# Kernel tuning notes

Hardware: AMD Instinct MI355X
Metric: run time of the kernel (lower is better)

Reference implementation:

```python
import jax, jax.numpy as jnp
import numpy as np


def setup_inputs() -> dict:
    key = jax.random.key(0)
    ks = jax.random.split(key, 6)
    m, d, n, p = 4096, 1024, 16, 1024  # tokens, input_dim, num_experts, output_dim (=slots)
    h = (d + p) * 2 // 3  # 1365, hidden_dim per original module
    s = 0.02
    return {
        "x": jax.random.normal(ks[0], (m, d), jnp.float32),
        "phi": jax.random.normal(ks[1], (d, n, p), jnp.float32) * s,
        "W1": jax.random.normal(ks[2], (n, d, h), jnp.float32) * s,
        "b1": jax.random.normal(ks[3], (n, h), jnp.float32) * s,
        "W2": jax.random.normal(ks[4], (n, h, p), jnp.float32) * s,
        "b2": jax.random.normal(ks[5], (n, p), jnp.float32) * s,
    }


def reference(x, phi, W1, b1, W2, b2):
    # logits: [m, n, p] = tokens x experts x slots
    logits = jnp.einsum('md,dnp->mnp', x, phi)
    # Dispatch weights: softmax over tokens' expert axis (dim=1 in torch == experts n)
    D = jax.nn.softmax(logits, axis=1)
    # Combine weights: softmax over all (expert, slot) pairs per token
    m = logits.shape[0]
    C = jax.nn.softmax(logits.reshape(m, -1), axis=-1).reshape(logits.shape)
    # Slot inputs: [n, p, d]
    Xs = jnp.einsum('md,mnp->npd', x, D)
    # Batched per-expert MLP (replaces the Python loop over experts)
    H = jax.nn.relu(jnp.einsum('npd,ndh->nph', Xs, W1) + b1[:, None, :])
    Ys = jnp.einsum('nph,nho->npo', H, W2) + b2[:, None, :]  # [n, p, out]
    # Combine: [m, out]; flatten(start_dim=1) on a 2D tensor is a no-op
    Y = jnp.einsum('npo,mnp->mo', Ys, C)
    return Y
```

## Files before the change

kernel.cpp:

```cpp
#include <hip/hip_runtime.h>
#include <math.h>

#define MTOK 4096
#define DDIM 1024
#define NEXP 16
#define PSLOT 1024
#define NPDIM 16384
#define HDIM 1365
#define HPAD 1376
#define KSPL 4

typedef unsigned short u16;
typedef __attribute__((ext_vector_type(8))) short short8;
typedef __attribute__((ext_vector_type(8))) unsigned short ushort8;
typedef __attribute__((ext_vector_type(2))) unsigned int uint32x2;
typedef __attribute__((ext_vector_type(4))) unsigned int uint32x4;
typedef __attribute__((ext_vector_type(4))) float f32x4;

template<bool Bc, typename T, typename F> struct cond_t { using type = T; };
template<typename T, typename F> struct cond_t<false, T, F> { using type = F; };

__device__ __forceinline__ float b2f(u16 v) {
    union { unsigned int u; float f; } x;
    x.u = ((unsigned int)v) << 16;
    return x.f;
}
__device__ __forceinline__ u16 f2b(float f) {
    union { float f; unsigned int u; } x;
    x.f = f;
    unsigned int r = x.u + 0x7FFFu + ((x.u >> 16) & 1u);
    return (u16)(r >> 16);
}
__device__ __forceinline__ unsigned int cvtpk(float lo, float hi) {
    unsigned int r;
    asm("v_cvt_pk_bf16_f32 %0, %1, %2" : "=v"(r) : "v"(lo), "v"(hi));
    return r;
}
__device__ __forceinline__ void stv(float* p, long long i, float v) { p[i] = v; }
__device__ __forceinline__ void stv(u16*  p, long long i, float v) { p[i] = f2b(v); }

template<int AMODE, int BMODE, typename TA, typename TB, typename TC,
         bool BIASF, bool RELUF, bool ROWSC, bool BCHK>
__global__ __launch_bounds__(512) void mgemm(
    const TA* __restrict__ A, long long sA, int lda,
    const TB* __restrict__ B, long long sB, int ldb,
    TC* __restrict__ C, long long sC, int ldc,
    const float* __restrict__ S,
    const float* __restrict__ bias, long long sBias,
    const float* __restrict__ rowsc,
    int M, int N, int NZ, int K, int Kb, int Nb)
{
    constexpr int AS = (AMODE == 0) ? 32 : 40;
    constexpr int BS = (BMODE == 0) ? 32 : 40;
    __shared__ u16 As[2][256 * AS];
    __shared__ u16 Bs[2][128 * BS];

    const int bz = blockIdx.z;
    A += (long long)bz * sA;
    B += (long long)bz * sB;
    C += (long long)bz * sC;
    const float* biasp = BIASF ? (bias + (long long)bz * sBias) : nullptr;

    const int gx = gridDim.x;
    const int nwg = gx * gridDim.y;
    int wg = blockIdx.x + gx * blockIdx.y;
    {
        const int q = nwg >> 3, r = nwg & 7, xc = wg & 7, ix = wg >> 3;
        wg = (xc < r ? xc * (q + 1) : r + xc * q) + ix;
    }
    const int m0 = (wg / gx) * 256;
    const int n0 = (wg % gx) * 128;

    const int tid  = threadIdx.x;
    const int lane = tid & 63;
    const int wv   = tid >> 6;
    const int wm   = wv & 3;
    const int wn   = wv >> 2;
    const int quad = lane >> 4;
    const int l16  = lane & 15;

    const int cla  = 2 * (tid & 127);
    const int k8a  = tid >> 7;
    const int clb  = 2 * (tid & 63);
    const int kqb  = tid >> 6;
    const int ngb  = n0 + clb;

    auto aoff = [&](int row, int k8) {
        int o = row * AS + k8 * 8;
        if constexpr (AMODE != 0) o ^= ((row >> 3) & 3) << 3;
        return o;
    };
    auto boff = [&](int row, int kel) {
        int o = row * BS + kel;
        if constexpr (BMODE != 0) o ^= ((row >> 3) & 3) << 3;
        return o;
    };

    f32x4 acc[4][4];
#pragma unroll
    for (int i = 0; i < 4; ++i)
#pragma unroll
        for (int j = 0; j < 4; ++j) acc[i][j] = (f32x4){0.f, 0.f, 0.f, 0.f};

    using BRAW = typename cond_t<sizeof(TB) == 2, unsigned int[4], float[8]>::type;

    auto LOADA0 = [&](int k0, int buf) {
#pragma unroll
        for (int q = 0; q < 2; ++q) {
            const u16* gp = A + (long long)(m0 + wv * 32 + q * 16 + (lane >> 2)) * lda
                              + k0 + (lane & 3) * 8;
            u16* lp = &As[buf][(wv * 32 + q * 16) * 32];
            __builtin_amdgcn_global_load_lds(
                (const __attribute__((address_space(1))) unsigned int*)gp,
                (__attribute__((address_space(3))) unsigned int*)lp, 16, 0, 0);
        }
    };
    auto LOADA2 = [&](int k0, unsigned int (&araw)[8], float2 (&sr)[8]) {
#pragma unroll
        for (int i = 0; i < 8; ++i) {
            const long long kg = k0 + k8a * 8 + i;
            araw[i] = *(const unsigned int*)((const u16*)A + kg * lda + (m0 + cla));
            sr[i]   = *(const float2*)&S[kg * 1024 + ((m0 + cla) & 1023)];
        }
    };
    auto WRITEA = [&](int buf, unsigned int (&araw)[8], float2 (&sr)[8]) {
        uint32x4 wa, wb;
#pragma unroll
        for (int j = 0; j < 4; ++j) {
            const unsigned int r0 = araw[2 * j], r1 = araw[2 * j + 1];
            wa[j] = cvtpk(b2f((u16)(r0 & 0xFFFFu)) * sr[2 * j].x,
                          b2f((u16)(r1 & 0xFFFFu)) * sr[2 * j + 1].x);
            wb[j] = cvtpk(b2f((u16)(r0 >> 16)) * sr[2 * j].y,
                          b2f((u16)(r1 >> 16)) * sr[2 * j + 1].y);
        }
        *(uint32x4*)&As[buf][aoff(cla, k8a)]     = wa;
        *(uint32x4*)&As[buf][aoff(cla + 1, k8a)] = wb;
    };
    auto LOADB0 = [&](int k0, int buf) {
        const u16* gp = (const u16*)B + (long long)(n0 + wv * 16 + (lane >> 2)) * ldb
                          + k0 + (lane & 3) * 8;
        u16* lp = &Bs[buf][(wv * 16) * 32];
        __builtin_amdgcn_global_load_lds(
            (const __attribute__((address_space(1))) unsigned int*)gp,
            (__attribute__((address_space(3))) unsigned int*)lp, 16, 0, 0);
    };
    auto LOADB = [&](int k0, BRAW& braw) {
        if constexpr (sizeof(TB) == 2) {
#pragma unroll
            for (int i = 0; i < 4; ++i) {
                const int kg = k0 + kqb * 4 + i;
                braw[i] = *(const unsigned int*)((const u16*)B + (long long)kg * ldb + ngb);
            }
        } else {
            bool full = true;
            if constexpr (BCHK) full = (k0 + 32 <= Kb) && (n0 + 128 <= Nb);
            if (full) {
#pragma unroll
                for (int i = 0; i < 4; ++i) {
                    const int kg = k0 + kqb * 4 + i;
                    const float* bp = (const float*)B + (long long)kg * ldb + ngb;
                    braw[2 * i]     = bp[0];
                    braw[2 * i + 1] = bp[1];
                }
            } else {
#pragma unroll
                for (int i = 0; i < 4; ++i) {
                    const int kg = k0 + kqb * 4 + i;
                    float v0 = 0.f, v1 = 0.f;
                    if (kg < Kb) {
                        if (ngb < Nb)     v0 = ((const float*)B)[(long long)kg * ldb + ngb];
                        if (ngb + 1 < Nb) v1 = ((const float*)B)[(long long)kg * ldb + ngb + 1];
                    }
                    braw[2 * i]     = v0;
                    braw[2 * i + 1] = v1;
                }
            }
        }
    };
    auto WRITEB = [&](int buf, BRAW& braw) {
        uint32x2 wa, wb;
        if constexpr (sizeof(TB) == 2) {
            wa[0] = (braw[0] & 0xFFFFu) | (braw[1] << 16);
            wa[1] = (braw[2] & 0xFFFFu) | (braw[3] << 16);
            wb[0] = (braw[0] >> 16) | (braw[1] & 0xFFFF0000u);
            wb[1] = (braw[2] >> 16) | (braw[3] & 0xFFFF0000u);
        } else {
            wa[0] = cvtpk(braw[0], braw[2]);
            wa[1] = cvtpk(braw[4], braw[6]);
            wb[0] = cvtpk(braw[1], braw[3]);
            wb[1] = cvtpk(braw[5], braw[7]);
        }
        *(uint32x2*)&Bs[buf][boff(clb, kqb * 4)]     = wa;
        *(uint32x2*)&Bs[buf][boff(clb + 1, kqb * 4)] = wb;
    };
    auto MM = [&](int buf) {
        short8 bfr[4];
#pragma unroll
        for (int ni = 0; ni < 4; ++ni)
            bfr[ni] = *(const short8*)&Bs[buf][boff(wn * 64 + ni * 16 + l16, quad * 8)];
#pragma unroll
        for (int mi = 0; mi < 4; ++mi) {
            short8 a = *(const short8*)&As[buf][aoff(wm * 64 + mi * 16 + l16, quad)];
#pragma unroll
            for (int ni = 0; ni < 4; ++ni)
                acc[mi][ni] = __builtin_amdgcn_mfma_f32_16x16x32_bf16(a, bfr[ni], acc[mi][ni], 0, 0, 0);
        }
    };

    const int nt = K >> 5;
    unsigned int a0[8];
    float2 sr[8];
    BRAW braw;
    {
        if constexpr (AMODE == 0) LOADA0(0, 0);
        else                      LOADA2(0, a0, sr);
        if constexpr (BMODE == 0) LOADB0(0, 0);
        else                      LOADB(0, braw);
        if constexpr (AMODE != 0) WRITEA(0, a0, sr);
        if constexpr (BMODE != 0) WRITEB(0, braw);
        __syncthreads();
    }
    for (int t = 0; t < nt; ++t) {
        const int cur = t & 1, nxt = cur ^ 1;
        const bool pf = (t + 1 < nt);
        if (pf) {
            if constexpr (AMODE == 0) LOADA0((t + 1) * 32, nxt);
            else                      LOADA2((t + 1) * 32, a0, sr);
            if constexpr (BMODE == 0) LOADB0((t + 1) * 32, nxt);
            else                      LOADB((t + 1) * 32, braw);
        }
        MM(cur);
        if (pf) {
            if constexpr (AMODE != 0) WRITEA(nxt, a0, sr);
            if constexpr (BMODE != 0) WRITEB(nxt, braw);
        }
        __syncthreads();
    }

#pragma unroll
    for (int mi = 0; mi < 4; ++mi) {
#pragma unroll
        for (int r = 0; r < 4; ++r) {
            const int rg = m0 + wm * 64 + mi * 16 + quad * 4 + r;
            if (rg >= M) continue;
            const float rs = ROWSC ? rowsc[rg] : 1.f;
#pragma unroll
            for (int ni = 0; ni < 4; ++ni) {
                const int cg = n0 + wn * 64 + ni * 16 + l16;
                if (cg < N) {
                    float v = acc[mi][ni][r];
                    if (BIASF) v += biasp[cg];
                    if (RELUF) v = fmaxf(v, 0.f);
                    if (ROWSC) v *= rs;
                    stv(C, (long long)rg * ldc + cg, v);
                } else if (cg < NZ) {
                    stv(C, (long long)rg * ldc + cg, 0.f);
                }
            }
        }
    }
}

__global__ __launch_bounds__(256) void cvt_k(
    const float* __restrict__ src, u16* __restrict__ dst, long long n)
{
    const long long i = ((long long)blockIdx.x * 256 + threadIdx.x) * 8;
    if (i >= n) return;
    const float4 a = *(const float4*)&src[i];
    const float4 b = *(const float4*)&src[i + 4];
    uint32x4 v;
    v[0] = cvtpk(a.x, a.y);
    v[1] = cvtpk(a.z, a.w);
    v[2] = cvtpk(b.x, b.y);
    v[3] = cvtpk(b.z, b.w);
    *(uint32x4*)&dst[i] = v;
}

__global__ __launch_bounds__(256) void tcvt_k(
    const float* __restrict__ src, u16* __restrict__ dst, int R, int C)
{
    __shared__ float t[32][33];
    const int c0 = blockIdx.x * 32, r0 = blockIdx.y * 32;
    const int tr = threadIdx.x >> 3;
    const int tc = (threadIdx.x & 7) * 4;
    const float4 v = *(const float4*)&src[(long long)(r0 + tr) * C + c0 + tc];
    t[tr][tc]     = v.x;
    t[tr][tc + 1] = v.y;
    t[tr][tc + 2] = v.z;
    t[tr][tc + 3] = v.w;
    __syncthreads();
    uint32x2 o;
    o[0] = cvtpk(t[tc][tr],     t[tc + 1][tr]);
    o[1] = cvtpk(t[tc + 2][tr], t[tc + 3][tr]);
    *(uint32x2*)&dst[(long long)(c0 + tr) * R + r0 + tc] = o;
}

__global__ __launch_bounds__(256) void softmax_k(
    u16* __restrict__ L, float* __restrict__ rsd, float* __restrict__ rsc)
{
    const int m = blockIdx.x;
    u16* row = L + (long long)m * NPDIM;
    const int tid = threadIdx.x;
    __shared__ float red[256];

    float mx = -1e30f;
    for (int i = tid * 8; i < NPDIM; i += 2048) {
        const ushort8 v = *(const ushort8*)&row[i];
#pragma unroll
        for (int j = 0; j < 8; ++j) mx = fmaxf(mx, b2f(v[j]));
    }
    red[tid] = mx;
    __syncthreads();
    for (int s = 128; s > 0; s >>= 1) {
        if (tid < s) red[tid] = fmaxf(red[tid], red[tid + s]);
        __syncthreads();
    }
    const float mxAll = red[0];
    __syncthreads();

    float sum = 0.f;
    for (int i = tid * 8; i < NPDIM; i += 2048) {
        const ushort8 v = *(const ushort8*)&row[i];
        ushort8 e;
#pragma unroll
        for (int j = 0; j < 8; ++j) {
            const float ef = __expf(b2f(v[j]) - mxAll);
            const u16 eb = f2b(ef);
            e[j] = eb;
            sum += b2f(eb);
        }
        *(ushort8*)&row[i] = e;
    }
    red[tid] = sum;
    __syncthreads();
    for (int s = 128; s > 0; s >>= 1) {
        if (tid < s) red[tid] += red[tid + s];
        __syncthreads();
    }
    if (tid == 0) rsc[m] = 1.f / red[0];
    __syncthreads();

    {
        const int p0 = tid * 4;
        float s0 = 0.f, s1 = 0.f, s2 = 0.f, s3 = 0.f;
#pragma unroll
        for (int n = 0; n < NEXP; ++n) {
            const ushort4 v = *(const ushort4*)&row[n * PSLOT + p0];
            s0 += b2f(v.x); s1 += b2f(v.y); s2 += b2f(v.z); s3 += b2f(v.w);
        }
        const float4 r = {1.f / s0, 1.f / s1, 1.f / s2, 1.f / s3};
        *(float4*)&rsd[(long long)m * PSLOT + p0] = r;
    }
}

__global__ __launch_bounds__(256) void reduce_k(
    const float* __restrict__ Yp, float* __restrict__ Y)
{
    const long long S = (long long)MTOK * PSLOT;
    const long long i = ((long long)blockIdx.x * 256 + threadIdx.x) * 4;
    f32x4 r = *(const f32x4*)&Yp[i];
#pragma unroll
    for (int z = 1; z < KSPL; ++z) r += *(const f32x4*)&Yp[(long long)z * S + i];
    *(f32x4*)&Y[i] = r;
}

extern "C" void kernel_launch(void* const* d_in, const int* in_sizes, int n_in,
                              void* d_out, int out_size, void* d_ws, size_t ws_size,
                              hipStream_t stream)
{
    const float* x   = (const float*)d_in[0];
    const float* phi = (const float*)d_in[1];
    const float* W1  = (const float*)d_in[2];
    const float* b1  = (const float*)d_in[3];
    const float* W2  = (const float*)d_in[4];
    const float* b2  = (const float*)d_in[5];
    float* Y = (float*)d_out;

    char* w = (char*)d_ws;
    u16*   L     = (u16*)w;   w += (size_t)MTOK * NPDIM * 2;
    u16*   Ys    = (u16*)w;   w += (size_t)NEXP * PSLOT * PSLOT * 2;
    float* rsc   = (float*)w; w += (size_t)MTOK * 4;
    float* Yp    = (float*)w;
    float* rsd   = (float*)w; w += (size_t)MTOK * PSLOT * 4;
    u16*   Xs    = (u16*)w;   w += (size_t)NEXP * PSLOT * DDIM * 2;
    u16*   Hb    = (u16*)w;   w += (size_t)NEXP * PSLOT * HPAD * 2;
    u16*   phibT = Ys;
    u16*   xb    = Hb;
    u16*   xbT   = Hb + (size_t)MTOK * DDIM;

    cvt_k<<<dim3((MTOK * DDIM) / (8 * 256)), 256, 0, stream>>>(x, xb, (long long)MTOK * DDIM);
    tcvt_k<<<dim3(DDIM / 32, MTOK / 32), 256, 0, stream>>>(x, xbT, MTOK, DDIM);
    tcvt_k<<<dim3(NPDIM / 32, DDIM / 32), 256, 0, stream>>>(phi, phibT, DDIM, NPDIM);

    mgemm<0, 0, u16, u16, u16, false, false, false, false>
        <<<dim3(NPDIM / 128, MTOK / 256, 1), 512, 0, stream>>>(
        xb, 0, DDIM,  phibT, 0, DDIM,  L, 0, NPDIM,
        nullptr, nullptr, 0, nullptr,
        MTOK, NPDIM, NPDIM, DDIM, DDIM, NPDIM);

    softmax_k<<<dim3(MTOK), 256, 0, stream>>>(L, rsd, rsc);

    mgemm<2, 0, u16, u16, u16, false, false, false, false>
        <<<dim3(DDIM / 128, NPDIM / 256, 1), 512, 0, stream>>>(
        L, 0, NPDIM,  xbT, 0, MTOK,  Xs, 0, DDIM,
        rsd, nullptr, 0, nullptr,
        NPDIM, DDIM, DDIM, MTOK, MTOK, DDIM);

    mgemm<0, 1, u16, float, u16, true, true, false, true>
        <<<dim3((HPAD + 127) / 128, PSLOT / 256, NEXP), 512, 0, stream>>>(
        Xs, (long long)PSLOT * DDIM, DDIM,
        W1, (long long)DDIM * HDIM, HDIM,
        Hb, (long long)PSLOT * HPAD, HPAD,
        nullptr, b1, HDIM, nullptr,
        PSLOT, HDIM, HPAD, DDIM, DDIM, HDIM);

    mgemm<0, 1, u16, float, u16, true, false, false, true>
        <<<dim3(PSLOT / 128, PSLOT / 256, NEXP), 512, 0, stream>>>(
        Hb, (long long)PSLOT * HPAD, HPAD,
        W2, (long long)HDIM * PSLOT, PSLOT,
        Ys, (long long)PSLOT * PSLOT, PSLOT,
        nullptr, b2, PSLOT, nullptr,
        PSLOT, PSLOT, PSLOT, HPAD, HDIM, PSLOT);

    mgemm<0, 1, u16, u16, float, false, false, true, false>
        <<<dim3(PSLOT / 128, MTOK / 256, KSPL), 512, 0, stream>>>(
        L, (long long)(NPDIM / KSPL), NPDIM,
        Ys, (long long)(NPDIM / KSPL) * PSLOT, PSLOT,
        Yp, (long long)MTOK * PSLOT, PSLOT,
        nullptr, nullptr, 0, rsc,
        MTOK, PSLOT, PSLOT, NPDIM / KSPL, NPDIM / KSPL, PSLOT);

    reduce_k<<<dim3((MTOK * PSLOT) / (4 * 256)), 256, 0, stream>>>(Yp, Y);
}
```

Baseline: 1.171 ms.

## Widen A/B staging loads to 4-element vectors and fuse x conversion kernels

The scaled-A staging path (AMODE 2) now loads 4 consecutive columns with one uint2 load and the matching scale vector with one f32x4 load, then writes four transposed rows to LDS. A new BAL4 variant loads fp32 B tiles with float4 loads for the W2 GEMM, replacing the scalar float loads. The two separate x conversion kernels (row-major and transposed bf16) are merged into one kernel that reads x once. The aim is fewer, wider global loads and one less pass over x. The price is a changed LDS write pattern and more per-thread repacking, which could cause bank conflicts.

```diff
diff --git a/kernel.cpp b/kernel.cpp
--- a/kernel.cpp
+++ b/kernel.cpp
@@ -20,6 +20,10 @@
 template<bool Bc, typename T, typename F> struct cond_t { using type = T; };
 template<typename T, typename F> struct cond_t<false, T, F> { using type = F; };
 
+struct b16raw  { unsigned int v[4]; };
+struct f32raw  { float v[8]; };
+struct f32raw4 { f32x4 v[2]; };
+
 __device__ __forceinline__ float b2f(u16 v) {
     union { unsigned int u; float f; } x;
     x.u = ((unsigned int)v) << 16;
@@ -40,7 +44,7 @@
 __device__ __forceinline__ void stv(u16*  p, long long i, float v) { p[i] = f2b(v); }
 
 template<int AMODE, int BMODE, typename TA, typename TB, typename TC,
-         bool BIASF, bool RELUF, bool ROWSC, bool BCHK>
+         bool BIASF, bool RELUF, bool ROWSC, bool BCHK, bool BAL4>
 __global__ __launch_bounds__(512) void mgemm(
     const TA* __restrict__ A, long long sA, int lda,
     const TB* __restrict__ B, long long sB, int ldb,
@@ -79,14 +83,16 @@
     const int quad = lane >> 4;
     const int l16  = lane & 15;
 
-    const int cla  = 2 * (tid & 127);
-    const int k8a  = tid >> 7;
+    const int cg4  = 4 * (tid & 63);
+    const int kg4  = (tid >> 6) * 4;
     const int clb  = 2 * (tid & 63);
     const int kqb  = tid >> 6;
     const int ngb  = n0 + clb;
-
-    auto aoff = [&](int row, int k8) {
-        int o = row * AS + k8 * 8;
+    const int cb4  = 4 * (tid & 31);
+    const int kb2  = (tid >> 5) * 2;
+
+    auto aoff = [&](int row, int kel) {
+        int o = row * AS + kel;
         if constexpr (AMODE != 0) o ^= ((row >> 3) & 3) << 3;
         return o;
     };
@@ -102,7 +108,8 @@
 #pragma unroll
         for (int j = 0; j < 4; ++j) acc[i][j] = (f32x4){0.f, 0.f, 0.f, 0.f};
 
-    using BRAW = typename cond_t<sizeof(TB) == 2, unsigned int[4], float[8]>::type;
+    using BRAW = typename cond_t<sizeof(TB) == 2, b16raw,
+                   typename cond_t<BAL4, f32raw4, f32raw>::type>::type;
 
     auto LOADA0 = [&](int k0, int buf) {
 #pragma unroll
@@ -115,26 +122,29 @@
                 (__attribute__((address_space(3))) unsigned int*)lp, 16, 0, 0);
         }
     };
-    auto LOADA2 = [&](int k0, unsigned int (&araw)[8], float2 (&sr)[8]) {
-#pragma unroll
-        for (int i = 0; i < 8; ++i) {
-            const long long kg = k0 + k8a * 8 + i;
-            araw[i] = *(const unsigned int*)((const u16*)A + kg * lda + (m0 + cla));
-            sr[i]   = *(const float2*)&S[kg * 1024 + ((m0 + cla) & 1023)];
-        }
-    };
-    auto WRITEA = [&](int buf, unsigned int (&araw)[8], float2 (&sr)[8]) {
-        uint32x4 wa, wb;
+    auto LOADA2 = [&](int k0, uint2 (&araw)[4], f32x4 (&sr)[4]) {
 #pragma unroll
         for (int j = 0; j < 4; ++j) {
-            const unsigned int r0 = araw[2 * j], r1 = araw[2 * j + 1];
-            wa[j] = cvtpk(b2f((u16)(r0 & 0xFFFFu)) * sr[2 * j].x,
-                          b2f((u16)(r1 & 0xFFFFu)) * sr[2 * j + 1].x);
-            wb[j] = cvtpk(b2f((u16)(r0 >> 16)) * sr[2 * j].y,
-                          b2f((u16)(r1 >> 16)) * sr[2 * j + 1].y);
-        }
-        *(uint32x4*)&As[buf][aoff(cla, k8a)]     = wa;
-        *(uint32x4*)&As[buf][aoff(cla + 1, k8a)] = wb;
+            const long long kg = k0 + kg4 + j;
+            araw[j] = *(const uint2*)((const u16*)A + kg * lda + (m0 + cg4));
+            sr[j]   = *(const f32x4*)&S[kg * 1024 + ((m0 + cg4) & 1023)];
+        }
+    };
+    auto WRITEA = [&](int buf, uint2 (&araw)[4], f32x4 (&sr)[4]) {
+#pragma unroll
+        for (int r = 0; r < 4; ++r) {
+            float e[4];
+#pragma unroll
+            for (int j = 0; j < 4; ++j) {
+                const unsigned int h = (r & 2) ? araw[j].y : araw[j].x;
+                const u16 b = (r & 1) ? (u16)(h >> 16) : (u16)(h & 0xFFFFu);
+                e[j] = b2f(b) * sr[j][r];
+            }
+            uint32x2 wp;
+            wp[0] = cvtpk(e[0], e[1]);
+            wp[1] = cvtpk(e[2], e[3]);
+            *(uint32x2*)&As[buf][aoff(cg4 + r, kg4)] = wp;
+        }
     };
     auto LOADB0 = [&](int k0, int buf) {
         const u16* gp = (const u16*)B + (long long)(n0 + wv * 16 + (lane >> 2)) * ldb
@@ -149,7 +159,34 @@
 #pragma unroll
             for (int i = 0; i < 4; ++i) {
                 const int kg = k0 + kqb * 4 + i;
-                braw[i] = *(const unsigned int*)((const u16*)B + (long long)kg * ldb + ngb);
+                braw.v[i] = *(const unsigned int*)((const u16*)B + (long long)kg * ldb + ngb);
+            }
+        } else if constexpr (BAL4) {
+            bool full = true;
+            if constexpr (BCHK) full = (k0 + 32 <= Kb) && (n0 + 128 <= Nb);
+            if (full) {
+#pragma unroll
+                for (int j = 0; j < 2; ++j) {
+                    const int kg = k0 + kb2 + j;
+                    braw.v[j] = *(const f32x4*)((const float*)B + (long long)kg * ldb + n0 + cb4);
+                }
+            } else {
+#pragma unroll
+                for (int j = 0; j < 2; ++j) {
+                    const int kg = k0 + kb2 + j;
+                    f32x4 f = (f32x4){0.f, 0.f, 0.f, 0.f};
+                    if (kg < Kb) {
+                        if (n0 + 128 <= Nb) {
+                            f = *(const f32x4*)((const float*)B + (long long)kg * ldb + n0 + cb4);
+                        } else {
+#pragma unroll
+                            for (int r = 0; r < 4; ++r)
+                                if (n0 + cb4 + r < Nb)
+                                    f[r] = ((const float*)B)[(long long)kg * ldb + n0 + cb4 + r];
+                        }
+                    }
+                    braw.v[j] = f;
+                }
             }
         } else {
             bool full = true;
@@ -159,8 +196,8 @@
                 for (int i = 0; i < 4; ++i) {
                     const int kg = k0 + kqb * 4 + i;
                     const float* bp = (const float*)B + (long long)kg * ldb + ngb;
-                    braw[2 * i]     = bp[0];
-                    braw[2 * i + 1] = bp[1];
+                    braw.v[2 * i]     = bp[0];
+                    braw.v[2 * i + 1] = bp[1];
                 }
             } else {
 #pragma unroll
@@ -171,27 +208,35 @@
                         if (ngb < Nb)     v0 = ((const float*)B)[(long long)kg * ldb + ngb];
                         if (ngb + 1 < Nb) v1 = ((const float*)B)[(long long)kg * ldb + ngb + 1];
                     }
-                    braw[2 * i]     = v0;
-                    braw[2 * i + 1] = v1;
+                    braw.v[2 * i]     = v0;
+                    braw.v[2 * i + 1] = v1;
                 }
             }
         }
     };
     auto WRITEB = [&](int buf, BRAW& braw) {
-        uint32x2 wa, wb;
         if constexpr (sizeof(TB) == 2) {
-            wa[0] = (braw[0] & 0xFFFFu) | (braw[1] << 16);
-            wa[1] = (braw[2] & 0xFFFFu) | (braw[3] << 16);
-            wb[0] = (braw[0] >> 16) | (braw[1] & 0xFFFF0000u);
-            wb[1] = (braw[2] >> 16) | (braw[3] & 0xFFFF0000u);
+            uint32x2 wa, wb;
+            wa[0] = (braw.v[0] & 0xFFFFu) | (braw.v[1] << 16);
+            wa[1] = (braw.v[2] & 0xFFFFu) | (braw.v[3] << 16);
+            wb[0] = (braw.v[0] >> 16) | (braw.v[1] & 0xFFFF0000u);
+            wb[1] = (braw.v[2] >> 16) | (braw.v[3] & 0xFFFF0000u);
+            *(uint32x2*)&Bs[buf][boff(clb, kqb * 4)]     = wa;
+            *(uint32x2*)&Bs[buf][boff(clb + 1, kqb * 4)] = wb;
+        } else if constexpr (BAL4) {
+#pragma unroll
+            for (int r = 0; r < 4; ++r)
+                *(unsigned int*)&Bs[buf][boff(cb4 + r, kb2)] =
+                    cvtpk(braw.v[0][r], braw.v[1][r]);
         } else {
-            wa[0] = cvtpk(braw[0], braw[2]);
-            wa[1] = cvtpk(braw[4], braw[6]);
-            wb[0] = cvtpk(braw[1], braw[3]);
-            wb[1] = cvtpk(braw[5], braw[7]);
-        }
-        *(uint32x2*)&Bs[buf][boff(clb, kqb * 4)]     = wa;
-        *(uint32x2*)&Bs[buf][boff(clb + 1, kqb * 4)] = wb;
+            uint32x2 wa, wb;
+            wa[0] = cvtpk(braw.v[0], braw.v[2]);
+            wa[1] = cvtpk(braw.v[4], braw.v[6]);
+            wb[0] = cvtpk(braw.v[1], braw.v[3]);
+            wb[1] = cvtpk(braw.v[5], braw.v[7]);
+            *(uint32x2*)&Bs[buf][boff(clb, kqb * 4)]     = wa;
+            *(uint32x2*)&Bs[buf][boff(clb + 1, kqb * 4)] = wb;
+        }
     };
     auto MM = [&](int buf) {
         short8 bfr[4];
@@ -200,7 +245,7 @@
             bfr[ni] = *(const short8*)&Bs[buf][boff(wn * 64 + ni * 16 + l16, quad * 8)];
 #pragma unroll
         for (int mi = 0; mi < 4; ++mi) {
-            short8 a = *(const short8*)&As[buf][aoff(wm * 64 + mi * 16 + l16, quad)];
+            short8 a = *(const short8*)&As[buf][aoff(wm * 64 + mi * 16 + l16, quad * 8)];
 #pragma unroll
             for (int ni = 0; ni < 4; ++ni)
                 acc[mi][ni] = __builtin_amdgcn_mfma_f32_16x16x32_bf16(a, bfr[ni], acc[mi][ni], 0, 0, 0);
@@ -208,8 +253,8 @@
     };
 
     const int nt = K >> 5;
-    unsigned int a0[8];
-    float2 sr[8];
+    uint2 a0[4];
+    f32x4 sr[4];
     BRAW braw;
     {
         if constexpr (AMODE == 0) LOADA0(0, 0);
@@ -261,19 +306,28 @@
     }
 }
 
-__global__ __launch_bounds__(256) void cvt_k(
-    const float* __restrict__ src, u16* __restrict__ dst, long long n)
-{
-    const long long i = ((long long)blockIdx.x * 256 + threadIdx.x) * 8;
-    if (i >= n) return;
-    const float4 a = *(const float4*)&src[i];
-    const float4 b = *(const float4*)&src[i + 4];
-    uint32x4 v;
-    v[0] = cvtpk(a.x, a.y);
-    v[1] = cvtpk(a.z, a.w);
-    v[2] = cvtpk(b.x, b.y);
-    v[3] = cvtpk(b.z, b.w);
-    *(uint32x4*)&dst[i] = v;
+__global__ __launch_bounds__(256) void xcvt_k(
+    const float* __restrict__ src, u16* __restrict__ dst_rm,
+    u16* __restrict__ dst_tr, int R, int C)
+{
+    __shared__ float t[32][33];
+    const int c0 = blockIdx.x * 32, r0 = blockIdx.y * 32;
+    const int tr = threadIdx.x >> 3;
+    const int tc = (threadIdx.x & 7) * 4;
+    const float4 v = *(const float4*)&src[(long long)(r0 + tr) * C + c0 + tc];
+    t[tr][tc]     = v.x;
+    t[tr][tc + 1] = v.y;
+    t[tr][tc + 2] = v.z;
+    t[tr][tc + 3] = v.w;
+    uint32x2 o1;
+    o1[0] = cvtpk(v.x, v.y);
+    o1[1] = cvtpk(v.z, v.w);
+    *(uint32x2*)&dst_rm[(long long)(r0 + tr) * C + c0 + tc] = o1;
+    __syncthreads();
+    uint32x2 o;
+    o[0] = cvtpk(t[tc][tr],     t[tc + 1][tr]);
+    o[1] = cvtpk(t[tc + 2][tr], t[tc + 3][tr]);
+    *(uint32x2*)&dst_tr[(long long)(c0 + tr) * R + r0 + tc] = o;
 }
 
 __global__ __launch_bounds__(256) void tcvt_k(
@@ -388,11 +442,10 @@
     u16*   xb    = Hb;
     u16*   xbT   = Hb + (size_t)MTOK * DDIM;
 
-    cvt_k<<<dim3((MTOK * DDIM) / (8 * 256)), 256, 0, stream>>>(x, xb, (long long)MTOK * DDIM);
-    tcvt_k<<<dim3(DDIM / 32, MTOK / 32), 256, 0, stream>>>(x, xbT, MTOK, DDIM);
+    xcvt_k<<<dim3(DDIM / 32, MTOK / 32), 256, 0, stream>>>(x, xb, xbT, MTOK, DDIM);
     tcvt_k<<<dim3(NPDIM / 32, DDIM / 32), 256, 0, stream>>>(phi, phibT, DDIM, NPDIM);
 
-    mgemm<0, 0, u16, u16, u16, false, false, false, false>
+    mgemm<0, 0, u16, u16, u16, false, false, false, false, false>
         <<<dim3(NPDIM / 128, MTOK / 256, 1), 512, 0, stream>>>(
         xb, 0, DDIM,  phibT, 0, DDIM,  L, 0, NPDIM,
         nullptr, nullptr, 0, nullptr,
@@ -400,13 +453,13 @@
 
     softmax_k<<<dim3(MTOK), 256, 0, stream>>>(L, rsd, rsc);
 
-    mgemm<2, 0, u16, u16, u16, false, false, false, false>
+    mgemm<2, 0, u16, u16, u16, false, false, false, false, false>
         <<<dim3(DDIM / 128, NPDIM / 256, 1), 512, 0, stream>>>(
         L, 0, NPDIM,  xbT, 0, MTOK,  Xs, 0, DDIM,
         rsd, nullptr, 0, nullptr,
         NPDIM, DDIM, DDIM, MTOK, MTOK, DDIM);
 
-    mgemm<0, 1, u16, float, u16, true, true, false, true>
+    mgemm<0, 1, u16, float, u16, true, true, false, true, false>
         <<<dim3((HPAD + 127) / 128, PSLOT / 256, NEXP), 512, 0, stream>>>(
         Xs, (long long)PSLOT * DDIM, DDIM,
         W1, (long long)DDIM * HDIM, HDIM,
@@ -414,7 +467,7 @@
         nullptr, b1, HDIM, nullptr,
         PSLOT, HDIM, HPAD, DDIM, DDIM, HDIM);
 
-    mgemm<0, 1, u16, float, u16, true, false, false, true>
+    mgemm<0, 1, u16, float, u16, true, false, false, true, true>
         <<<dim3(PSLOT / 128, PSLOT / 256, NEXP), 512, 0, stream>>>(
         Hb, (long long)PSLOT * HPAD, HPAD,
         W2, (long long)HDIM * PSLOT, PSLOT,
@@ -422,7 +475,7 @@
         nullptr, b2, PSLOT, nullptr,
         PSLOT, PSLOT, PSLOT, HPAD, HDIM, PSLOT);
 
-    mgemm<0, 1, u16, u16, float, false, false, true, false>
+    mgemm<0, 1, u16, u16, float, false, false, true, false, false>
         <<<dim3(PSLOT / 128, MTOK / 256, KSPL), 512, 0, stream>>>(
         L, (long long)(NPDIM / KSPL), NPDIM,
         Ys, (long long)(NPDIM / KSPL) * PSLOT, PSLOT,
```

Measured after the change: 1.150 ms. About the same (-1.8%).
